# Performance work log

Measured on AMD Instinct MI355X. Metric: run time of the kernel, lower is better.

## Reference

```python
import jax, jax.numpy as jnp
import numpy as np

NUM_CLASSES = 1000
K_PROTOS = 5
FEAT_DIM = 1024
BATCH = 16384


def _l2norm(x, axis=-1, eps=1e-12):
    # matches torch.nn.functional.normalize
    n = jnp.linalg.norm(x, axis=axis, keepdims=True)
    return x / jnp.maximum(n, eps)


def setup_inputs() -> dict:
    key = jax.random.key(0)
    k1, k2, k3 = jax.random.split(key, 3)
    z = jax.random.normal(k1, (BATCH, FEAT_DIM), dtype=jnp.float32)
    y = jax.random.randint(k2, (BATCH,), 0, NUM_CLASSES, dtype=jnp.int64)
    # learned prototype bank, dense [C, K, D] (all slots populated)
    P = jax.random.normal(k3, (NUM_CLASSES, K_PROTOS, FEAT_DIM), dtype=jnp.float32)
    return {"z": z, "y": y, "P": P}


def reference(z, y, P):
    """Returns (pos_sim [B], neg_sim [B]): max cosine sim to same-class and
    other-class prototypes respectively (PrototypeBank.forward)."""
    C, K, D = P.shape
    z_n = _l2norm(z)                     # [B, D]
    P_n = _l2norm(P).reshape(C * K, D)   # [C*K, D]
    sim = jnp.einsum('bd,pd->bp', z_n, P_n)  # [B, C*K]
    proto_labels = jnp.repeat(jnp.arange(C, dtype=y.dtype), K)  # [C*K]
    same = proto_labels[None, :] == y[:, None]  # [B, C*K]
    neg_inf = jnp.asarray(-jnp.inf, sim.dtype)
    pos_sim = jnp.max(jnp.where(same, sim, neg_inf), axis=1)
    neg_sim = jnp.max(jnp.where(same, neg_inf, sim), axis=1)
    return pos_sim, neg_sim
```

## Files before the change

### kernel.cpp

```cpp
#include <hip/hip_runtime.h>
#include <hip/hip_bf16.h>
#include <stdint.h>

#define BATCH 16384
#define D 1024
#define NCLS 1000
#define NPROTO 5000
#define NPROTO_PAD 5120
#define BM 64
#define NCH 10
#define NKT 32
#define KSTRIDE (320 * 64 * 8)

typedef float f32x4 __attribute__((ext_vector_type(4)));
typedef __bf16 bf16x8 __attribute__((ext_vector_type(8)));

__device__ __forceinline__ unsigned short f2bf(float x) {
    unsigned u = __float_as_uint(x);
    u += 0x7FFFu + ((u >> 16) & 1u);
    return (unsigned short)(u >> 16);
}

__global__ __launch_bounds__(256) void k_prep(
        const float* __restrict__ z, const float* __restrict__ P,
        unsigned short* __restrict__ zb, unsigned short* __restrict__ pbf) {
    const int b = blockIdx.x;
    const int t = threadIdx.x;
    const int e0 = 4 * t;
    const float* src = nullptr;
    unsigned short* dst;
    if (b < BATCH) {
        src = z + (size_t)b * D;
        dst = zb + (size_t)b * D + e0;
    } else {
        const int r = b - BATCH;
        const int kt = e0 >> 5;
        const int lk = (e0 >> 3) & 3;
        const int ke = e0 & 7;
        dst = pbf + (((size_t)kt * 320 + (r >> 4)) * 64 + (r & 15) + 16 * lk) * 8 + ke;
        if (r < NPROTO) src = P + (size_t)r * D;
    }
    if (src == nullptr) {
        *(ushort4*)dst = make_ushort4(0, 0, 0, 0);
        return;
    }
    float4 v = ((const float4*)src)[t];
    float ss = v.x * v.x + v.y * v.y + v.z * v.z + v.w * v.w;
    #pragma unroll
    for (int o = 32; o >= 1; o >>= 1) ss += __shfl_xor(ss, o);
    __shared__ float red[4];
    const int wave = t >> 6;
    if ((t & 63) == 0) red[wave] = ss;
    __syncthreads();
    const float s = red[0] + red[1] + red[2] + red[3];
    const float inv = 1.0f / fmaxf(sqrtf(s), 1e-12f);
    ushort4 o4;
    o4.x = f2bf(v.x * inv); o4.y = f2bf(v.y * inv);
    o4.z = f2bf(v.z * inv); o4.w = f2bf(v.w * inv);
    *(ushort4*)dst = o4;
}

#define MM(A, B, C) __builtin_amdgcn_mfma_f32_16x16x32_bf16(A, B, C, 0, 0, 0)

__global__ __launch_bounds__(1024, 4) void k_gemm(
        const unsigned short* __restrict__ zb,
        const unsigned short* __restrict__ pbf,
        const int* __restrict__ y,
        float* __restrict__ out) {
    __shared__ __align__(16) unsigned short LA[NKT][4][64][8];
    __shared__ float redP[16][64];
    __shared__ float redN[16][64];

    const int t = threadIdx.x;
    const int w = t >> 6;
    const int lane = t & 63;
    const int lm = lane & 15, lk = lane >> 4;
    const int rowbase = blockIdx.x * BM;

    {
        const int ktw = lane >> 1;
        const int lk0 = (lane & 1) * 2;
        #pragma unroll
        for (int j = 0; j < 4; ++j) {
            const int r = w * 4 + j;
            const unsigned short* gp = zb + (size_t)(rowbase + r) * D + lane * 16;
            const bf16x8 v0 = *(const bf16x8*)gp;
            const bf16x8 v1 = *(const bf16x8*)(gp + 8);
            *(bf16x8*)&LA[ktw][r >> 4][(r & 15) + 16 * lk0][0] = v0;
            *(bf16x8*)&LA[ktw][r >> 4][(r & 15) + 16 * (lk0 + 1)][0] = v1;
        }
    }
    int yv[16];
    #pragma unroll
    for (int mi = 0; mi < 4; ++mi)
        #pragma unroll
        for (int r = 0; r < 4; ++r)
            yv[mi * 4 + r] = y[rowbase + mi * 16 + lk * 4 + r];

    __syncthreads();

    float pmv[16], nmv[16];
    #pragma unroll
    for (int i = 0; i < 16; ++i) { pmv[i] = -INFINITY; nmv[i] = -INFINITY; }

    for (int c = 0; c < NCH; ++c) {
        const int grp0 = c * 32 + w * 2;
        const unsigned short* pB = pbf + ((size_t)grp0 * 64 + lane) * 8;

        f32x4 acc[4][2];
        #pragma unroll
        for (int mi = 0; mi < 4; ++mi)
            #pragma unroll
            for (int ni = 0; ni < 2; ++ni) {
                f32x4 z4 = {0.0f, 0.0f, 0.0f, 0.0f};
                acc[mi][ni] = z4;
            }

        bf16x8 b00 = *(const bf16x8*)(pB);
        bf16x8 b01 = *(const bf16x8*)(pB + 512);
        bf16x8 b10 = *(const bf16x8*)(pB + KSTRIDE);
        bf16x8 b11 = *(const bf16x8*)(pB + KSTRIDE + 512);

        #pragma unroll 1
        for (int kt = 0; kt < NKT; kt += 2) {
            {
                const bf16x8 a0 = *(const bf16x8*)&LA[kt][0][lane][0];
                const bf16x8 a1 = *(const bf16x8*)&LA[kt][1][lane][0];
                const bf16x8 a2 = *(const bf16x8*)&LA[kt][2][lane][0];
                const bf16x8 a3 = *(const bf16x8*)&LA[kt][3][lane][0];
                acc[0][0] = MM(a0, b00, acc[0][0]);
                acc[0][1] = MM(a0, b01, acc[0][1]);
                acc[1][0] = MM(a1, b00, acc[1][0]);
                acc[1][1] = MM(a1, b01, acc[1][1]);
                acc[2][0] = MM(a2, b00, acc[2][0]);
                acc[2][1] = MM(a2, b01, acc[2][1]);
                acc[3][0] = MM(a3, b00, acc[3][0]);
                acc[3][1] = MM(a3, b01, acc[3][1]);
                const int ktn = (kt + 2 < NKT) ? kt + 2 : NKT - 1;
                b00 = *(const bf16x8*)(pB + (size_t)ktn * KSTRIDE);
                b01 = *(const bf16x8*)(pB + (size_t)ktn * KSTRIDE + 512);
            }
            {
                const bf16x8 a0 = *(const bf16x8*)&LA[kt + 1][0][lane][0];
                const bf16x8 a1 = *(const bf16x8*)&LA[kt + 1][1][lane][0];
                const bf16x8 a2 = *(const bf16x8*)&LA[kt + 1][2][lane][0];
                const bf16x8 a3 = *(const bf16x8*)&LA[kt + 1][3][lane][0];
                acc[0][0] = MM(a0, b10, acc[0][0]);
                acc[0][1] = MM(a0, b11, acc[0][1]);
                acc[1][0] = MM(a1, b10, acc[1][0]);
                acc[1][1] = MM(a1, b11, acc[1][1]);
                acc[2][0] = MM(a2, b10, acc[2][0]);
                acc[2][1] = MM(a2, b11, acc[2][1]);
                acc[3][0] = MM(a3, b10, acc[3][0]);
                acc[3][1] = MM(a3, b11, acc[3][1]);
                const int ktn = (kt + 3 < NKT) ? kt + 3 : NKT - 1;
                b10 = *(const bf16x8*)(pB + (size_t)ktn * KSTRIDE);
                b11 = *(const bf16x8*)(pB + (size_t)ktn * KSTRIDE + 512);
            }
        }

        #pragma unroll
        for (int ni = 0; ni < 2; ++ni) {
            const unsigned col = (unsigned)(c * 512 + w * 32 + ni * 16 + lm);
            const unsigned lbl = __umulhi(col, 0xCCCCCCCDu) >> 2;
            const bool valid = col < NPROTO;
            #pragma unroll
            for (int mi = 0; mi < 4; ++mi)
                #pragma unroll
                for (int r = 0; r < 4; ++r) {
                    const float v = acc[mi][ni][r];
                    const bool same = (lbl == (unsigned)yv[mi * 4 + r]);
                    const int i = mi * 4 + r;
                    pmv[i] = same ? fmaxf(pmv[i], v) : pmv[i];
                    nmv[i] = (!same && valid) ? fmaxf(nmv[i], v) : nmv[i];
                }
        }
    }

    #pragma unroll
    for (int i = 0; i < 16; ++i) {
        #pragma unroll
        for (int off = 1; off < 16; off <<= 1) {
            pmv[i] = fmaxf(pmv[i], __shfl_xor(pmv[i], off));
            nmv[i] = fmaxf(nmv[i], __shfl_xor(nmv[i], off));
        }
    }
    if (lm == 0) {
        #pragma unroll
        for (int mi = 0; mi < 4; ++mi)
            #pragma unroll
            for (int r = 0; r < 4; ++r) {
                redP[w][mi * 16 + lk * 4 + r] = pmv[mi * 4 + r];
                redN[w][mi * 16 + lk * 4 + r] = nmv[mi * 4 + r];
            }
    }
    __syncthreads();
    if (t < 64) {
        float p = redP[0][t], n = redN[0][t];
        #pragma unroll
        for (int ww = 1; ww < 16; ++ww) {
            p = fmaxf(p, redP[ww][t]);
            n = fmaxf(n, redN[ww][t]);
        }
        out[rowbase + t] = p;
        out[BATCH + rowbase + t] = n;
    }
}

extern "C" void kernel_launch(void* const* d_in, const int* in_sizes, int n_in,
                              void* d_out, int out_size, void* d_ws, size_t ws_size,
                              hipStream_t stream) {
    const float* z = (const float*)d_in[0];
    const int*   y = (const int*)d_in[1];
    const float* P = (const float*)d_in[2];

    unsigned short* zb = (unsigned short*)d_ws;
    unsigned short* pbf = zb + (size_t)BATCH * D;
    float* out = (float*)d_out;

    k_prep<<<BATCH + NPROTO_PAD, 256, 0, stream>>>(z, P, zb, pbf);
    k_gemm<<<BATCH / BM, 1024, 0, stream>>>(zb, pbf, y, out);
}
```

Baseline: 188.4 us.

## Widen per-wave prototype tile to 64 columns and halve chunk count

Each wave now computes a 64x64 output tile (four 16-column groups) per chunk instead of 64x32, so every LDS A-fragment read feeds 16 MFMAs instead of 8, and the number of chunks drops from 10 to 5. The B-operand prefetch is restructured: the next k-step's four fragments load at the top of each iteration, and the current buffer reloads between the two MFMA halves. This cuts LDS traffic and loop overhead per FLOP, at the cost of doubling accumulator and B registers, which may hurt occupancy under launch_bounds(1024,4).

```diff
diff --git a/kernel.cpp b/kernel.cpp
--- a/kernel.cpp
+++ b/kernel.cpp
@@ -8,7 +8,7 @@
 #define NPROTO 5000
 #define NPROTO_PAD 5120
 #define BM 64
-#define NCH 10
+#define NCH 5
 #define NKT 32
 #define KSTRIDE (320 * 64 * 8)
 
@@ -103,65 +103,92 @@
     #pragma unroll
     for (int i = 0; i < 16; ++i) { pmv[i] = -INFINITY; nmv[i] = -INFINITY; }
 
+    #pragma unroll 1
     for (int c = 0; c < NCH; ++c) {
-        const int grp0 = c * 32 + w * 2;
+        const int grp0 = c * 64 + w * 4;
         const unsigned short* pB = pbf + ((size_t)grp0 * 64 + lane) * 8;
 
-        f32x4 acc[4][2];
+        f32x4 acc[4][4];
         #pragma unroll
         for (int mi = 0; mi < 4; ++mi)
             #pragma unroll
-            for (int ni = 0; ni < 2; ++ni) {
+            for (int ni = 0; ni < 4; ++ni) {
                 f32x4 z4 = {0.0f, 0.0f, 0.0f, 0.0f};
                 acc[mi][ni] = z4;
             }
 
-        bf16x8 b00 = *(const bf16x8*)(pB);
-        bf16x8 b01 = *(const bf16x8*)(pB + 512);
-        bf16x8 b10 = *(const bf16x8*)(pB + KSTRIDE);
-        bf16x8 b11 = *(const bf16x8*)(pB + KSTRIDE + 512);
+        bf16x8 bc0 = *(const bf16x8*)(pB);
+        bf16x8 bc1 = *(const bf16x8*)(pB + 512);
+        bf16x8 bc2 = *(const bf16x8*)(pB + 1024);
+        bf16x8 bc3 = *(const bf16x8*)(pB + 1536);
+        bf16x8 bn0, bn1, bn2, bn3;
 
         #pragma unroll 1
         for (int kt = 0; kt < NKT; kt += 2) {
+            {
+                const unsigned short* q = pB + (size_t)(kt + 1) * KSTRIDE;
+                bn0 = *(const bf16x8*)(q);
+                bn1 = *(const bf16x8*)(q + 512);
+                bn2 = *(const bf16x8*)(q + 1024);
+                bn3 = *(const bf16x8*)(q + 1536);
+            }
             {
                 const bf16x8 a0 = *(const bf16x8*)&LA[kt][0][lane][0];
                 const bf16x8 a1 = *(const bf16x8*)&LA[kt][1][lane][0];
                 const bf16x8 a2 = *(const bf16x8*)&LA[kt][2][lane][0];
                 const bf16x8 a3 = *(const bf16x8*)&LA[kt][3][lane][0];
-                acc[0][0] = MM(a0, b00, acc[0][0]);
-                acc[0][1] = MM(a0, b01, acc[0][1]);
-                acc[1][0] = MM(a1, b00, acc[1][0]);
-                acc[1][1] = MM(a1, b01, acc[1][1]);
-                acc[2][0] = MM(a2, b00, acc[2][0]);
-                acc[2][1] = MM(a2, b01, acc[2][1]);
-                acc[3][0] = MM(a3, b00, acc[3][0]);
-                acc[3][1] = MM(a3, b01, acc[3][1]);
+                acc[0][0] = MM(a0, bc0, acc[0][0]);
+                acc[0][1] = MM(a0, bc1, acc[0][1]);
+                acc[0][2] = MM(a0, bc2, acc[0][2]);
+                acc[0][3] = MM(a0, bc3, acc[0][3]);
+                acc[1][0] = MM(a1, bc0, acc[1][0]);
+                acc[1][1] = MM(a1, bc1, acc[1][1]);
+                acc[1][2] = MM(a1, bc2, acc[1][2]);
+                acc[1][3] = MM(a1, bc3, acc[1][3]);
+                acc[2][0] = MM(a2, bc0, acc[2][0]);
+                acc[2][1] = MM(a2, bc1, acc[2][1]);
+                acc[2][2] = MM(a2, bc2, acc[2][2]);
+                acc[2][3] = MM(a2, bc3, acc[2][3]);
+                acc[3][0] = MM(a3, bc0, acc[3][0]);
+                acc[3][1] = MM(a3, bc1, acc[3][1]);
+                acc[3][2] = MM(a3, bc2, acc[3][2]);
+                acc[3][3] = MM(a3, bc3, acc[3][3]);
+            }
+            {
                 const int ktn = (kt + 2 < NKT) ? kt + 2 : NKT - 1;
-                b00 = *(const bf16x8*)(pB + (size_t)ktn * KSTRIDE);
-                b01 = *(const bf16x8*)(pB + (size_t)ktn * KSTRIDE + 512);
+                const unsigned short* q = pB + (size_t)ktn * KSTRIDE;
+                bc0 = *(const bf16x8*)(q);
+                bc1 = *(const bf16x8*)(q + 512);
+                bc2 = *(const bf16x8*)(q + 1024);
+                bc3 = *(const bf16x8*)(q + 1536);
             }
             {
                 const bf16x8 a0 = *(const bf16x8*)&LA[kt + 1][0][lane][0];
                 const bf16x8 a1 = *(const bf16x8*)&LA[kt + 1][1][lane][0];
                 const bf16x8 a2 = *(const bf16x8*)&LA[kt + 1][2][lane][0];
                 const bf16x8 a3 = *(const bf16x8*)&LA[kt + 1][3][lane][0];
-                acc[0][0] = MM(a0, b10, acc[0][0]);
-                acc[0][1] = MM(a0, b11, acc[0][1]);
-                acc[1][0] = MM(a1, b10, acc[1][0]);
-                acc[1][1] = MM(a1, b11, acc[1][1]);
-                acc[2][0] = MM(a2, b10, acc[2][0]);
-                acc[2][1] = MM(a2, b11, acc[2][1]);
-                acc[3][0] = MM(a3, b10, acc[3][0]);
-                acc[3][1] = MM(a3, b11, acc[3][1]);
-                const int ktn = (kt + 3 < NKT) ? kt + 3 : NKT - 1;
-                b10 = *(const bf16x8*)(pB + (size_t)ktn * KSTRIDE);
-                b11 = *(const bf16x8*)(pB + (size_t)ktn * KSTRIDE + 512);
-            }
-        }
-
-        #pragma unroll
-        for (int ni = 0; ni < 2; ++ni) {
-            const unsigned col = (unsigned)(c * 512 + w * 32 + ni * 16 + lm);
+                acc[0][0] = MM(a0, bn0, acc[0][0]);
+                acc[0][1] = MM(a0, bn1, acc[0][1]);
+                acc[0][2] = MM(a0, bn2, acc[0][2]);
+                acc[0][3] = MM(a0, bn3, acc[0][3]);
+                acc[1][0] = MM(a1, bn0, acc[1][0]);
+                acc[1][1] = MM(a1, bn1, acc[1][1]);
+                acc[1][2] = MM(a1, bn2, acc[1][2]);
+                acc[1][3] = MM(a1, bn3, acc[1][3]);
+                acc[2][0] = MM(a2, bn0, acc[2][0]);
+                acc[2][1] = MM(a2, bn1, acc[2][1]);
+                acc[2][2] = MM(a2, bn2, acc[2][2]);
+                acc[2][3] = MM(a2, bn3, acc[2][3]);
+                acc[3][0] = MM(a3, bn0, acc[3][0]);
+                acc[3][1] = MM(a3, bn1, acc[3][1]);
+                acc[3][2] = MM(a3, bn2, acc[3][2]);
+                acc[3][3] = MM(a3, bn3, acc[3][3]);
+            }
+        }
+
+        #pragma unroll
+        for (int ni = 0; ni < 4; ++ni) {
+            const unsigned col = (unsigned)(c * 1024 + w * 64 + ni * 16 + lm);
             const unsigned lbl = __umulhi(col, 0xCCCCCCCDu) >> 2;
             const bool valid = col < NPROTO;
             #pragma unroll
```

After: 180.9 us. 4.0% less time.

## Widen per-wave prototype tile to 64 columns and reduce per chunk

Applied to the files above, without the earlier changes.

Each wave now computes a 64x64 tile (four 16-column B fragments) per chunk instead of 64x32, so each LDS A-fragment load feeds twice as many MFMAs and the chunk count halves. The register-prefetched B double-buffer is replaced by plain loads at the top of each k-step. The pos/neg max reduction moves inside the chunk loop and accumulates through shared memory, so 32 running-max registers are no longer held across chunks. This frees registers for the larger accumulator tile, at the cost of exposed global-load latency on B and extra shuffles and LDS writes per chunk.

```diff
diff --git a/kernel.cpp b/kernel.cpp
--- a/kernel.cpp
+++ b/kernel.cpp
@@ -8,7 +8,7 @@
 #define NPROTO 5000
 #define NPROTO_PAD 5120
 #define BM 64
-#define NCH 10
+#define NCH 5
 #define NKT 32
 #define KSTRIDE (320 * 64 * 8)
 
@@ -77,6 +77,9 @@
     const int lm = lane & 15, lk = lane >> 4;
     const int rowbase = blockIdx.x * BM;
 
+    redP[t >> 6][t & 63] = -INFINITY;
+    redN[t >> 6][t & 63] = -INFINITY;
+
     {
         const int ktw = lane >> 1;
         const int lk0 = (lane & 1) * 2;
@@ -90,110 +93,80 @@
             *(bf16x8*)&LA[ktw][r >> 4][(r & 15) + 16 * (lk0 + 1)][0] = v1;
         }
     }
-    int yv[16];
-    #pragma unroll
-    for (int mi = 0; mi < 4; ++mi)
-        #pragma unroll
-        for (int r = 0; r < 4; ++r)
-            yv[mi * 4 + r] = y[rowbase + mi * 16 + lk * 4 + r];
-
     __syncthreads();
 
-    float pmv[16], nmv[16];
-    #pragma unroll
-    for (int i = 0; i < 16; ++i) { pmv[i] = -INFINITY; nmv[i] = -INFINITY; }
-
+    #pragma unroll 1
     for (int c = 0; c < NCH; ++c) {
-        const int grp0 = c * 32 + w * 2;
+        const int grp0 = c * 64 + w * 4;
         const unsigned short* pB = pbf + ((size_t)grp0 * 64 + lane) * 8;
 
-        f32x4 acc[4][2];
+        f32x4 acc[4][4];
         #pragma unroll
         for (int mi = 0; mi < 4; ++mi)
             #pragma unroll
-            for (int ni = 0; ni < 2; ++ni) {
+            for (int ni = 0; ni < 4; ++ni) {
                 f32x4 z4 = {0.0f, 0.0f, 0.0f, 0.0f};
                 acc[mi][ni] = z4;
             }
 
-        bf16x8 b00 = *(const bf16x8*)(pB);
-        bf16x8 b01 = *(const bf16x8*)(pB + 512);
-        bf16x8 b10 = *(const bf16x8*)(pB + KSTRIDE);
-        bf16x8 b11 = *(const bf16x8*)(pB + KSTRIDE + 512);
-
         #pragma unroll 1
-        for (int kt = 0; kt < NKT; kt += 2) {
-            {
-                const bf16x8 a0 = *(const bf16x8*)&LA[kt][0][lane][0];
-                const bf16x8 a1 = *(const bf16x8*)&LA[kt][1][lane][0];
-                const bf16x8 a2 = *(const bf16x8*)&LA[kt][2][lane][0];
-                const bf16x8 a3 = *(const bf16x8*)&LA[kt][3][lane][0];
-                acc[0][0] = MM(a0, b00, acc[0][0]);
-                acc[0][1] = MM(a0, b01, acc[0][1]);
-                acc[1][0] = MM(a1, b00, acc[1][0]);
-                acc[1][1] = MM(a1, b01, acc[1][1]);
-                acc[2][0] = MM(a2, b00, acc[2][0]);
-                acc[2][1] = MM(a2, b01, acc[2][1]);
-                acc[3][0] = MM(a3, b00, acc[3][0]);
-                acc[3][1] = MM(a3, b01, acc[3][1]);
-                const int ktn = (kt + 2 < NKT) ? kt + 2 : NKT - 1;
-                b00 = *(const bf16x8*)(pB + (size_t)ktn * KSTRIDE);
-                b01 = *(const bf16x8*)(pB + (size_t)ktn * KSTRIDE + 512);
-            }
-            {
-                const bf16x8 a0 = *(const bf16x8*)&LA[kt + 1][0][lane][0];
-                const bf16x8 a1 = *(const bf16x8*)&LA[kt + 1][1][lane][0];
-                const bf16x8 a2 = *(const bf16x8*)&LA[kt + 1][2][lane][0];
-                const bf16x8 a3 = *(const bf16x8*)&LA[kt + 1][3][lane][0];
-                acc[0][0] = MM(a0, b10, acc[0][0]);
-                acc[0][1] = MM(a0, b11, acc[0][1]);
-                acc[1][0] = MM(a1, b10, acc[1][0]);
-                acc[1][1] = MM(a1, b11, acc[1][1]);
-                acc[2][0] = MM(a2, b10, acc[2][0]);
-                acc[2][1] = MM(a2, b11, acc[2][1]);
-                acc[3][0] = MM(a3, b10, acc[3][0]);
-                acc[3][1] = MM(a3, b11, acc[3][1]);
-                const int ktn = (kt + 3 < NKT) ? kt + 3 : NKT - 1;
-                b10 = *(const bf16x8*)(pB + (size_t)ktn * KSTRIDE);
-                b11 = *(const bf16x8*)(pB + (size_t)ktn * KSTRIDE + 512);
-            }
+        for (int kt = 0; kt < NKT; ++kt) {
+            const unsigned short* q = pB + (size_t)kt * KSTRIDE;
+            const bf16x8 b0 = *(const bf16x8*)(q);
+            const bf16x8 b1 = *(const bf16x8*)(q + 512);
+            const bf16x8 b2 = *(const bf16x8*)(q + 1024);
+            const bf16x8 b3 = *(const bf16x8*)(q + 1536);
+            const bf16x8 a0 = *(const bf16x8*)&LA[kt][0][lane][0];
+            const bf16x8 a1 = *(const bf16x8*)&LA[kt][1][lane][0];
+            const bf16x8 a2 = *(const bf16x8*)&LA[kt][2][lane][0];
+            const bf16x8 a3 = *(const bf16x8*)&LA[kt][3][lane][0];
+            acc[0][0] = MM(a0, b0, acc[0][0]);
+            acc[0][1] = MM(a0, b1, acc[0][1]);
+            acc[0][2] = MM(a0, b2, acc[0][2]);
+            acc[0][3] = MM(a0, b3, acc[0][3]);
+            acc[1][0] = MM(a1, b0, acc[1][0]);
+            acc[1][1] = MM(a1, b1, acc[1][1]);
+            acc[1][2] = MM(a1, b2, acc[1][2]);
+            acc[1][3] = MM(a1, b3, acc[1][3]);
+            acc[2][0] = MM(a2, b0, acc[2][0]);
+            acc[2][1] = MM(a2, b1, acc[2][1]);
+            acc[2][2] = MM(a2, b2, acc[2][2]);
+            acc[2][3] = MM(a2, b3, acc[2][3]);
+            acc[3][0] = MM(a3, b0, acc[3][0]);
+            acc[3][1] = MM(a3, b1, acc[3][1]);
+            acc[3][2] = MM(a3, b2, acc[3][2]);
+            acc[3][3] = MM(a3, b3, acc[3][3]);
         }
 
         #pragma unroll
-        for (int ni = 0; ni < 2; ++ni) {
-            const unsigned col = (unsigned)(c * 512 + w * 32 + ni * 16 + lm);
-            const unsigned lbl = __umulhi(col, 0xCCCCCCCDu) >> 2;
-            const bool valid = col < NPROTO;
+        for (int mi = 0; mi < 4; ++mi) {
             #pragma unroll
-            for (int mi = 0; mi < 4; ++mi)
+            for (int r = 0; r < 4; ++r) {
+                const int row = mi * 16 + lk * 4 + r;
+                const unsigned yv = (unsigned)y[rowbase + row];
+                float pm = -INFINITY, nm = -INFINITY;
                 #pragma unroll
-                for (int r = 0; r < 4; ++r) {
+                for (int ni = 0; ni < 4; ++ni) {
+                    const unsigned col = (unsigned)(c * 1024 + w * 64 + ni * 16 + lm);
+                    const unsigned lbl = __umulhi(col, 0xCCCCCCCDu) >> 2;
                     const float v = acc[mi][ni][r];
-                    const bool same = (lbl == (unsigned)yv[mi * 4 + r]);
-                    const int i = mi * 4 + r;
-                    pmv[i] = same ? fmaxf(pmv[i], v) : pmv[i];
-                    nmv[i] = (!same && valid) ? fmaxf(nmv[i], v) : nmv[i];
+                    const bool same = (lbl == yv);
+                    pm = same ? fmaxf(pm, v) : pm;
+                    nm = (!same && col < NPROTO) ? fmaxf(nm, v) : nm;
                 }
+                #pragma unroll
+                for (int off = 1; off < 16; off <<= 1) {
+                    pm = fmaxf(pm, __shfl_xor(pm, off));
+                    nm = fmaxf(nm, __shfl_xor(nm, off));
+                }
+                if (lm == 0) {
+                    redP[w][row] = fmaxf(redP[w][row], pm);
+                    redN[w][row] = fmaxf(redN[w][row], nm);
+                }
+            }
         }
     }
 
-    #pragma unroll
-    for (int i = 0; i < 16; ++i) {
-        #pragma unroll
-        for (int off = 1; off < 16; off <<= 1) {
-            pmv[i] = fmaxf(pmv[i], __shfl_xor(pmv[i], off));
-            nmv[i] = fmaxf(nmv[i], __shfl_xor(nmv[i], off));
-        }
-    }
-    if (lm == 0) {
-        #pragma unroll
-        for (int mi = 0; mi < 4; ++mi)
-            #pragma unroll
-            for (int r = 0; r < 4; ++r) {
-                redP[w][mi * 16 + lk * 4 + r] = pmv[mi * 4 + r];
-                redN[w][mi * 16 + lk * 4 + r] = nmv[mi * 4 + r];
-            }
-    }
     __syncthreads();
     if (t < 64) {
         float p = redP[0][t], n = redN[0][t];
```

Result: faster. 181.1 us (-3.9%).
